# Kernel optimization log

Hardware: AMD Instinct MI355X
Metric: run time of the kernel (lower is better)

## Reference

```python
import jax, jax.numpy as jnp
import numpy as np

DIM = 1024
HEADS = 16
HEAD_DIM = DIM // HEADS
DFF = 4 * DIM  # SwiGLU expansion=4.0
EPS = 1e-5
NEG = -1e4  # original uses -1e4 causal mask, not -inf


def rms_norm(x, w):
    v = jnp.mean(x * x, axis=-1, keepdims=True)
    return w * (x * jax.lax.rsqrt(v + EPS))


def rotate_half(x):
    x1, x2 = jnp.split(x, 2, axis=-1)
    return jnp.concatenate((-x2, x1), axis=-1)


def setup_inputs() -> dict:
    key = jax.random.key(0)
    ks = jax.random.split(key, 12)
    B, S = 2, 2048
    s = 0.02
    h = jax.random.normal(ks[0], (B, S, DIM), jnp.float32)
    # RoPE tables, half-split convention: emb = concat(freqs, freqs)
    inv_freq = 1.0 / (10000.0 ** (np.arange(0, HEAD_DIM, 2, dtype=np.float32) / HEAD_DIM))
    freqs = np.arange(S, dtype=np.float32)[:, None] * inv_freq[None, :]
    emb = np.concatenate([freqs, freqs], axis=-1)
    cos = jnp.asarray(np.cos(emb))  # [S, HEAD_DIM]
    sin = jnp.asarray(np.sin(emb))
    return {
        "h": h, "cos": cos, "sin": sin,
        "norm1_w": jnp.ones((DIM,), jnp.float32),
        "wq": jax.random.normal(ks[1], (DIM, DIM), jnp.float32) * s,
        "wk": jax.random.normal(ks[2], (DIM, DIM), jnp.float32) * s,
        "wv": jax.random.normal(ks[3], (DIM, DIM), jnp.float32) * s,
        "wo": jax.random.normal(ks[4], (DIM, DIM), jnp.float32) * s,
        "norm2_w": jnp.ones((DIM,), jnp.float32),
        "gate_w": jax.random.normal(ks[5], (DFF, DIM), jnp.float32) * s,
        "gate_b": jnp.zeros((DFF,), jnp.float32),
        "up_w": jax.random.normal(ks[6], (DFF, DIM), jnp.float32) * s,
        "up_b": jnp.zeros((DFF,), jnp.float32),
        "down_w": jax.random.normal(ks[7], (DIM, DFF), jnp.float32) * s,
        "down_b": jnp.zeros((DIM,), jnp.float32),
        "gate": jnp.full((DIM,), 0.5, jnp.float32),
    }


def reference(h, cos, sin, norm1_w, wq, wk, wv, wo, norm2_w,
              gate_w, gate_b, up_w, up_b, down_w, down_b, gate):
    B, S, _ = h.shape
    scale = HEAD_DIM ** -0.5

    x = rms_norm(h, norm1_w)

    def heads(t):  # [B,S,DIM] -> [B,H,S,D]
        return t.reshape(B, S, HEADS, HEAD_DIM).transpose(0, 2, 1, 3)

    q = heads(x @ wq.T)
    k = heads(x @ wk.T)
    v = heads(x @ wv.T)

    # inline RoPE (cos/sin broadcast [S,D] over [B,H,S,D])
    q = q * cos + rotate_half(q) * sin
    k = k * cos + rotate_half(k) * sin

    scores = jnp.einsum('bhsd,bhtd->bhst', q, k) * scale
    causal = jnp.triu(jnp.full((S, S), NEG, jnp.float32), k=1)
    scores = scores + causal
    attn = jax.nn.softmax(scores, axis=-1)
    out = jnp.einsum('bhst,bhtd->bhsd', attn, v)
    out = out.transpose(0, 2, 1, 3).reshape(B, S, DIM)
    attn_out = out @ wo.T

    h = h + attn_out

    x2 = rms_norm(h, norm2_w)
    g = jax.nn.silu(x2 @ gate_w.T + gate_b)
    u = x2 @ up_w.T + up_b
    mlp = (g * u) @ down_w.T + down_b

    h = h + jax.nn.sigmoid(gate) * mlp
    return h
```

## Files before the change

### kernel.cpp

```cpp
#include <hip/hip_runtime.h>
#include <math.h>

#define DIM    1024
#define HEADS  16
#define HD     64
#define SEQ    2048
#define BATCH  2
#define TTOK   4096
#define DFF    4096
#define S3     3072
#define NTSW   16

typedef __attribute__((ext_vector_type(8))) short short8;
typedef __attribute__((ext_vector_type(4))) float f32x4;

__device__ __forceinline__ float bf2f(unsigned short u) {
  union { unsigned int u; float f; } v; v.u = ((unsigned int)u) << 16; return v.f;
}
__device__ __forceinline__ unsigned short f2bf(float f) {
  union { float f; unsigned int u; } v; v.f = f;
  return (unsigned short)((v.u + 0x7FFFu + ((v.u >> 16) & 1u)) >> 16);
}
__device__ __forceinline__ unsigned short f2bf_trunc(float f) {
  union { float f; unsigned int u; } v; v.f = f;
  return (unsigned short)(v.u >> 16);
}

#define AS1(p) ((const __attribute__((address_space(1))) void*)(p))
#define AS3(p) ((__attribute__((address_space(3))) void*)(p))

__global__ __launch_bounds__(256) void wconv_k(
    const float* __restrict__ s0, const float* __restrict__ s1,
    const float* __restrict__ s2, const float* __restrict__ s3,
    const float* __restrict__ s4, const float* __restrict__ s5,
    const float* __restrict__ s6, unsigned short* __restrict__ dst)
{
  const int i = blockIdx.x * 256 + threadIdx.x;
  const float* s; int base; int di = i;
  if (i < 1048576) {
    if (i < 524288) { if (i < 262144) { s = s0; base = 0; } else { s = s1; base = 262144; } }
    else            { if (i < 786432) { s = s2; base = 524288; } else { s = s3; base = 786432; } }
  } else if (i < 2097152) {
    s = s4; base = 1048576;
    const int u = i - base; const int r = u >> 8; const int c = u & 255;
    di = 1048576 + (((r >> 4) << 5) + (r & 15)) * 256 + c;
  } else if (i < 3145728) {
    s = s5; base = 2097152;
    const int u = i - base; const int r = u >> 8; const int c = u & 255;
    di = 1048576 + (((r >> 4) << 5) + 16 + (r & 15)) * 256 + c;
  } else {
    s = s6; base = 3145728;
  }
  const float4 f = ((const float4*)s)[i - base];
  unsigned long long o = (unsigned long long)f2bf(f.x)
                       | ((unsigned long long)f2bf(f.y) << 16)
                       | ((unsigned long long)f2bf(f.z) << 32)
                       | ((unsigned long long)f2bf(f.w) << 48);
  ((unsigned long long*)dst)[di] = o;
}

template<int MODE>
__global__ __launch_bounds__(256) void gemm_bt(
    const unsigned short* __restrict__ A,
    const unsigned short* __restrict__ W,
    unsigned short* __restrict__ C,
    float* __restrict__ Cf,
    const float* __restrict__ resf,
    const float* __restrict__ cosp,
    const float* __restrict__ sinp,
    int M, int N, int K)
{
  __shared__ __align__(16) unsigned short As[128 * 64];
  __shared__ __align__(16) unsigned short Bs[128 * 64];

  const int tid  = threadIdx.x;
  const int lane = tid & 63;
  const int wv   = tid >> 6;
  const int row0 = blockIdx.x * 128;
  const int col0 = blockIdx.y * 128;
  const int wm   = (wv >> 1) * 64;
  const int wn   = (wv & 1) * 64;
  const int lr   = lane & 15;
  const int lg   = lane >> 4;

  const int srow = lane >> 3;
  const int skg  = (lane & 7) ^ srow;

  f32x4 acc[4][4];
#pragma unroll
  for (int i = 0; i < 4; i++)
#pragma unroll
    for (int j = 0; j < 4; j++) acc[i][j] = (f32x4){0.f, 0.f, 0.f, 0.f};

  for (int k0 = 0; k0 < K; k0 += 64) {
#pragma unroll
    for (int i = 0; i < 4; i++) {
      const int c = wv * 4 + i;
      const unsigned short* ga = A + (size_t)(row0 + c * 8 + srow) * K + k0 + skg * 8;
      __builtin_amdgcn_global_load_lds(AS1(ga), AS3(As + c * 512), 16, 0, 0);
      const unsigned short* gb = W + (size_t)(col0 + c * 8 + srow) * K + k0 + skg * 8;
      __builtin_amdgcn_global_load_lds(AS1(gb), AS3(Bs + c * 512), 16, 0, 0);
    }
    __syncthreads();

#pragma unroll
    for (int ks = 0; ks < 2; ks++) {
      short8 af[4], bf[4];
#pragma unroll
      for (int i = 0; i < 4; i++) {
        const int r = wm + i * 16 + lr;
        af[i] = *(const short8*)(As + r * 64 + (((ks * 4 + lg) ^ (lr & 7)) * 8));
      }
#pragma unroll
      for (int j = 0; j < 4; j++) {
        const int r = wn + j * 16 + lr;
        bf[j] = *(const short8*)(Bs + r * 64 + (((ks * 4 + lg) ^ (lr & 7)) * 8));
      }
#pragma unroll
      for (int i = 0; i < 4; i++)
#pragma unroll
        for (int j = 0; j < 4; j++)
          acc[i][j] = __builtin_amdgcn_mfma_f32_16x16x32_bf16(af[i], bf[j], acc[i][j], 0, 0, 0);
    }
    __syncthreads();
  }

  if (MODE == 5) {
    const bool do_rope = (col0 < 2048);
#pragma unroll
    for (int i = 0; i < 4; i++) {
#pragma unroll
      for (int r = 0; r < 4; r++) {
        const int row = row0 + wm + i * 16 + lg * 4 + r;
        const int s = row & (SEQ - 1);
        const size_t rb = (size_t)row * N + col0 + wn;
        if (do_rope) {
#pragma unroll
          for (int jp = 0; jp < 2; jp++) {
            const int d = jp * 16 + lr;
            const float c = cosp[s * HD + d];
            const float sn = sinp[s * HD + d];
            const float x1v = acc[i][jp][r];
            const float x2v = acc[i][jp + 2][r];
            C[rb + d]      = f2bf(x1v * c - x2v * sn);
            C[rb + d + 32] = f2bf(x2v * c + x1v * sn);
          }
        } else {
#pragma unroll
          for (int j = 0; j < 4; j++)
            C[rb + j * 16 + lr] = f2bf(acc[i][j][r]);
        }
      }
    }
    return;
  }

#pragma unroll
  for (int i = 0; i < 4; i++) {
#pragma unroll
    for (int j = 0; j < 4; j++) {
      const int col = col0 + wn + j * 16 + lr;
#pragma unroll
      for (int r = 0; r < 4; r++) {
        const int row = row0 + wm + i * 16 + lg * 4 + r;
        const float v = acc[i][j][r];
        const size_t idx = (size_t)row * N + col;
        if (MODE == 3) {
          Cf[idx] = v + resf[idx];
        }
      }
    }
  }
}

template<int MODE>
__global__ __launch_bounds__(512, 2) void gemm256_k(
    const unsigned short* __restrict__ A,
    const unsigned short* __restrict__ W,
    unsigned short* __restrict__ G,
    const float* __restrict__ gbias,
    const float* __restrict__ ubias,
    int Kst)
{
  __shared__ __align__(16) unsigned short Asl[2 * 16384];
  __shared__ __align__(16) unsigned short Bsl[2 * 16384];

  const int tid  = threadIdx.x;
  const int lane = tid & 63;
  const int wv   = tid >> 6;
  const int row0 = blockIdx.x * 256;
  const int col0 = blockIdx.y * 256;
  const int wm   = (wv >> 2) * 128;
  const int wn   = (wv & 3) * 64;
  const int lr   = lane & 15;
  const int lg   = lane >> 4;
  const int kb   = (MODE == 6) ? blockIdx.z * 1024 : 0;

  const int rl   = tid >> 3;
  const int rq   = (rl & 31) + ((rl >> 5) << 7);
  const int cl8  = ((tid & 7) ^ (rl & 7)) * 8;
  const int ldsu = wv * 512;

  auto stA = [&](int t, int q) {
    const unsigned short* s = A + (size_t)(row0 + q * 32 + rq) * Kst + kb + t * 64 + cl8;
    __builtin_amdgcn_global_load_lds(AS1(s), AS3(Asl + (t & 1) * 16384 + q * 4096 + ldsu), 16, 0, 0);
  };
  auto stB = [&](int t, int q) {
    const unsigned short* s = W + (size_t)(col0 + q * 32 + rq) * Kst + kb + t * 64 + cl8;
    __builtin_amdgcn_global_load_lds(AS1(s), AS3(Bsl + (t & 1) * 16384 + q * 4096 + ldsu), 16, 0, 0);
  };

  f32x4 acc[8][4];
#pragma unroll
  for (int f = 0; f < 8; f++)
#pragma unroll
    for (int j = 0; j < 4; j++) acc[f][j] = (f32x4){0.f, 0.f, 0.f, 0.f};

  stB(0, 0); stB(0, 1); stB(0, 2); stB(0, 3);
  stA(0, 0); stA(0, 1); stA(0, 2); stA(0, 3);
  stB(1, 0); stB(1, 1); stB(1, 2); stB(1, 3);
  stA(1, 0); stA(1, 1);
  asm volatile("s_waitcnt vmcnt(6)" ::: "memory");
  __builtin_amdgcn_s_barrier();

#pragma unroll 1
  for (int J = 0; J < NTSW / 2; ++J) {
    const int t2 = 2 * J + 2, t3 = 2 * J + 3;
#pragma unroll
    for (int h = 0; h < 2; ++h) {
      const unsigned short* Ab = Asl + h * 16384;
      const unsigned short* Bb = Bsl + h * 16384;
      short8 bfr[4][2];
#pragma unroll
      for (int p = 0; p < 4; ++p) {
        if (p == 0) {
#pragma unroll
          for (int j = 0; j < 4; ++j) {
            const int rn   = wn + j * 16 + lr;
            const int q    = (rn & 127) >> 5;
            const int rloc = (rn & 31) + ((rn >> 7) << 5);
#pragma unroll
            for (int ks = 0; ks < 2; ++ks)
              bfr[j][ks] = *(const short8*)(Bb + q * 4096 + rloc * 64 +
                                            (((ks * 4 + lg) ^ (lr & 7)) * 8));
          }
        }
        short8 af[2][2];
#pragma unroll
        for (int e = 0; e < 2; ++e) {
          const int rloc = e * 16 + lr + ((wv >> 2) << 5);
#pragma unroll
          for (int ks = 0; ks < 2; ++ks)
            af[e][ks] = *(const short8*)(Ab + p * 4096 + rloc * 64 +
                                         (((ks * 4 + lg) ^ (lr & 7)) * 8));
        }
        if (h == 0) {
          if (p == 0)      { stA(2 * J + 1, 2); stA(2 * J + 1, 3); }
          else if (p == 1) { if (t2 < NTSW) { stB(t2, 0); stB(t2, 1); } }
          else if (p == 2) { if (t2 < NTSW) { stB(t2, 2); stB(t2, 3); } }
          else {
            if (t2 < NTSW) { stA(t2, 0); stA(t2, 1);
                             asm volatile("s_waitcnt vmcnt(6)" ::: "memory"); }
            else           { asm volatile("s_waitcnt vmcnt(0)" ::: "memory"); }
          }
        } else {
          if (p == 0)      { if (t2 < NTSW) { stA(t2, 2); stA(t2, 3); } }
          else if (p == 1) { if (t3 < NTSW) { stB(t3, 0); stB(t3, 1); } }
          else if (p == 2) { if (t3 < NTSW) { stB(t3, 2); stB(t3, 3); } }
          else {
            if (t3 < NTSW) { stA(t3, 0); stA(t3, 1);
                             asm volatile("s_waitcnt vmcnt(6)" ::: "memory"); }
            else           { asm volatile("s_waitcnt vmcnt(0)" ::: "memory"); }
          }
        }
        __builtin_amdgcn_s_barrier();
        asm volatile("s_waitcnt lgkmcnt(0)" ::: "memory");
        __builtin_amdgcn_sched_barrier(0);
        __builtin_amdgcn_s_setprio(1);
#pragma unroll
        for (int e = 0; e < 2; ++e)
#pragma unroll
          for (int j = 0; j < 4; ++j)
#pragma unroll
            for (int ks = 0; ks < 2; ++ks)
              acc[2 * p + e][j] = __builtin_amdgcn_mfma_f32_16x16x32_bf16(
                  af[e][ks], bfr[j][ks], acc[2 * p + e][j], 0, 0, 0);
        __builtin_amdgcn_s_setprio(0);
        __builtin_amdgcn_s_barrier();
      }
    }
  }

  if (MODE == 7) {
    const int cb = (col0 + wn) >> 1;
#pragma unroll
    for (int jp = 0; jp < 2; ++jp) {
      const int lcol = cb + jp * 16 + lr;
      const float gbv = gbias[lcol];
      const float ubv = ubias[lcol];
#pragma unroll
      for (int f = 0; f < 8; ++f) {
#pragma unroll
        for (int r = 0; r < 4; ++r) {
          const int row = row0 + wm + f * 16 + lg * 4 + r;
          float gv = acc[f][2 * jp][r] + gbv;
          gv = gv / (1.0f + __expf(-gv));
          const float uv = acc[f][2 * jp + 1][r] + ubv;
          G[(size_t)row * DFF + lcol] = f2bf(gv * uv);
        }
      }
    }
  } else {
    const size_t pz[4] = {4u * 1048576u, 8u * 1048576u, 16u * 1048576u, 0u};
    unsigned short* Cz = G + pz[blockIdx.z];
#pragma unroll
    for (int j = 0; j < 4; ++j) {
      const int col = col0 + wn + j * 16 + lr;
#pragma unroll
      for (int f = 0; f < 8; ++f) {
#pragma unroll
        for (int r = 0; r < 4; ++r) {
          const int row = row0 + wm + f * 16 + lg * 4 + r;
          Cz[(size_t)row * DIM + col] = f2bf(acc[f][j][r]);
        }
      }
    }
  }
}

__global__ __launch_bounds__(256) void dcomb_k(
    const unsigned short* __restrict__ ws, float* __restrict__ out,
    const float* __restrict__ db, const float* __restrict__ gate)
{
  const int i4 = blockIdx.x * 256 + threadIdx.x;
  const size_t idx = (size_t)i4 * 4;
  const int col = (int)(idx & 1023);
  const unsigned long long p0 = *(const unsigned long long*)(ws + 4u * 1048576u + idx);
  const unsigned long long p1 = *(const unsigned long long*)(ws + 8u * 1048576u + idx);
  const unsigned long long p2 = *(const unsigned long long*)(ws + 16u * 1048576u + idx);
  const unsigned long long p3 = *(const unsigned long long*)(ws + idx);
  float4 o = *(float4*)(out + idx);
  float* op = (float*)&o;
#pragma unroll
  for (int w = 0; w < 4; w++) {
    const float s = bf2f((unsigned short)(p0 >> (16 * w)))
                  + bf2f((unsigned short)(p1 >> (16 * w)))
                  + bf2f((unsigned short)(p2 >> (16 * w)))
                  + bf2f((unsigned short)(p3 >> (16 * w)))
                  + db[col + w];
    const float sg = 1.0f / (1.0f + __expf(-gate[col + w]));
    op[w] += sg * s;
  }
  *(float4*)(out + idx) = o;
}

template<int XF32>
__global__ __launch_bounds__(256) void rmsnorm_k(
    const void* __restrict__ Xv,
    const float* __restrict__ W,
    unsigned short* __restrict__ Y)
{
  const int t  = blockIdx.x;
  const int i0 = threadIdx.x * 4;

  float v[4];
  if (XF32) {
    const float4 f = *(const float4*)((const float*)Xv + (size_t)t * DIM + i0);
    v[0] = f.x; v[1] = f.y; v[2] = f.z; v[3] = f.w;
  } else {
    unsigned long long raw = *(const unsigned long long*)((const unsigned short*)Xv + (size_t)t * DIM + i0);
#pragma unroll
    for (int k = 0; k < 4; k++) v[k] = bf2f((unsigned short)(raw >> (16 * k)));
  }

  float ss = v[0] * v[0] + v[1] * v[1] + v[2] * v[2] + v[3] * v[3];
#pragma unroll
  for (int off = 32; off > 0; off >>= 1) ss += __shfl_xor(ss, off);

  __shared__ float red[4];
  if ((threadIdx.x & 63) == 0) red[threadIdx.x >> 6] = ss;
  __syncthreads();
  const float tot = red[0] + red[1] + red[2] + red[3];
  const float r = rsqrtf(tot * (1.0f / DIM) + 1e-5f);

  const float4 wf = *(const float4*)(W + i0);
  const float wv4[4] = {wf.x, wf.y, wf.z, wf.w};
  unsigned long long o = 0;
#pragma unroll
  for (int k = 0; k < 4; k++)
    o |= ((unsigned long long)f2bf(v[k] * r * wv4[k])) << (16 * k);
  *(unsigned long long*)(Y + (size_t)t * DIM + i0) = o;
}

__device__ const unsigned char cqt[32] = {10,10,15,15,9,9,13,14,14,14,15,4,8,8,12,12,13,13,7,7,11,11,11,12,3,6,6,5,5,2,1,0};
__device__ const unsigned char ctb[32] = {0,11,0,11,0,10,0,0,10,20,22,0,0,9,0,9,10,19,0,8,0,8,16,18,0,0,7,0,6,0,0,0};
__device__ const unsigned char ccnt[32] = {11,11,11,11,10,10,10,10,10,10,10,10,9,9,9,9,9,9,8,8,8,8,8,8,8,7,7,6,6,6,4,2};
__device__ const unsigned char cchv[32] = {0,1,0,1,0,1,0,0,1,2,2,0,0,1,0,1,1,2,0,1,0,1,2,2,0,0,1,0,1,0,0,0};
__device__ const unsigned char cpsv[32] = {255,5,255,14,255,4,255,255,12,13,15,255,255,3,255,8,10,11,255,2,255,6,7,9,255,255,1,255,0,255,255,255};

__global__ __launch_bounds__(256) void fattn_k(
    const unsigned short* __restrict__ QKV,
    unsigned short* __restrict__ O,
    unsigned short* __restrict__ Pbuf,
    float* __restrict__ Lbuf)
{
  __shared__ __align__(16) unsigned short Ks[2][64 * 64];
  __shared__ __align__(16) unsigned short Vt[2][64 * 72];
  __shared__ __align__(16) unsigned short Ps[4 * 32 * 72];

  const int tid  = threadIdx.x;
  const int lane = tid & 63;
  const int wv   = tid >> 6;
  const int lr   = lane & 15;
  const int lg   = lane >> 4;

  const int j  = blockIdx.x;
  const int bh = blockIdx.y;
  const int qt = cqt[j];
  const int tb = ctb[j];
  const int nt = ccnt[j];
  const int ch = cchv[j];
  const int ps = cpsv[j];
  const int b  = bh >> 4, h = bh & 15;
  const int q0 = qt * 128;
  const size_t rowb = (size_t)b * SEQ;
  const int qoff = h * HD;
  const int koff = 1024 + qoff;
  const int voff = 2048 + qoff;

  short8 aq[2][2];
#pragma unroll
  for (int rf = 0; rf < 2; rf++) {
    const size_t tok = rowb + q0 + wv * 32 + rf * 16 + lr;
    aq[rf][0] = *(const short8*)(QKV + tok * S3 + qoff + lg * 8);
    aq[rf][1] = *(const short8*)(QKV + tok * S3 + qoff + 32 + lg * 8);
  }

  f32x4 o[2][4];
  f32x4 lacc[2];
#pragma unroll
  for (int rf = 0; rf < 2; rf++) {
    lacc[rf] = (f32x4){0.f, 0.f, 0.f, 0.f};
#pragma unroll
    for (int d = 0; d < 4; d++) o[rf][d] = (f32x4){0.f, 0.f, 0.f, 0.f};
  }
  short8 onesb;
#pragma unroll
  for (int jj = 0; jj < 8; jj++) onesb[jj] = (short)0x3F80;

  const int srow = lane >> 3;
  const int skg  = (lane & 7) ^ srow;
  const int kv   = tid >> 2;
  const int d0   = (tid & 3) * 16;

  const float C1 = 0.125f * 1.44269504f;
  const float C2 = 11.5415603f;

  auto stage = [&](int buf, int ti) {
    const int t0 = (tb + ti) * 64;
    unsigned short* ksb = &Ks[buf][0];
#pragma unroll
    for (int i = 0; i < 2; i++) {
      const int c = wv * 2 + i;
      const unsigned short* gk = QKV + (rowb + t0 + c * 8 + srow) * S3 + koff + skg * 8;
      __builtin_amdgcn_global_load_lds(AS1(gk), AS3(ksb + c * 512), 16, 0, 0);
    }
    unsigned short* vtb = &Vt[buf][0];
    const unsigned short* gv = QKV + (rowb + t0 + kv) * S3 + voff + d0;
    const short8 v0 = *(const short8*)gv;
    const short8 v1 = *(const short8*)(gv + 8);
    const int klo = kv & 7, khi = kv >> 3;
#pragma unroll
    for (int w = 0; w < 8; w++) {
      const int da = d0 + w, db2 = d0 + 8 + w;
      vtb[da  * 72 + ((khi ^ ((da  >> 3) & 7)) * 8) + klo] = (unsigned short)v0[w];
      vtb[db2 * 72 + ((khi ^ ((db2 >> 3) & 7)) * 8) + klo] = (unsigned short)v1[w];
    }
  };

  stage(0, 0);

  for (int ti = 0; ti < nt; ti++) {
    __syncthreads();
    if (ti + 1 < nt) stage((ti + 1) & 1, ti + 1);

    const int t0 = (tb + ti) * 64;
    const unsigned short* ksb = &Ks[ti & 1][0];
    const unsigned short* vtb = &Vt[ti & 1][0];

    f32x4 S[2][4];
#pragma unroll
    for (int sub = 0; sub < 4; sub++) {
      const int kr = sub * 16 + lr;
      const short8 bk0 = *(const short8*)(ksb + kr * 64 + ((lg       ^ (kr & 7)) * 8));
      const short8 bk1 = *(const short8*)(ksb + kr * 64 + (((4 + lg) ^ (kr & 7)) * 8));
#pragma unroll
      for (int rf = 0; rf < 2; rf++) {
        f32x4 s = (f32x4){0.f, 0.f, 0.f, 0.f};
        s = __builtin_amdgcn_mfma_f32_16x16x32_bf16(aq[rf][0], bk0, s, 0, 0, 0);
        s = __builtin_amdgcn_mfma_f32_16x16x32_bf16(aq[rf][1], bk1, s, 0, 0, 0);
        S[rf][sub] = s;
      }
    }

    unsigned short* pw = Ps + wv * (32 * 72);
#pragma unroll
    for (int rf = 0; rf < 2; rf++) {
      const int qmin = q0 + wv * 32 + rf * 16;
      const bool diag = (t0 + 63 > qmin);
#pragma unroll
      for (int sub = 0; sub < 4; sub++) {
#pragma unroll
        for (int r = 0; r < 4; r++) {
          float t = fmaf(S[rf][sub][r], C1, -C2);
          if (diag && (t0 + sub * 16 + lr > qmin + lg * 4 + r)) t = -INFINITY;
          const float p = exp2f(t);
          pw[(rf * 16 + lg * 4 + r) * 72 + sub * 16 + lr] = f2bf_trunc(p);
        }
      }
    }

#pragma unroll
    for (int kf = 0; kf < 2; kf++) {
      const short8 pa0 = *(const short8*)(pw + lr * 72 + kf * 32 + lg * 8);
      const short8 pa1 = *(const short8*)(pw + (16 + lr) * 72 + kf * 32 + lg * 8);
      lacc[0] = __builtin_amdgcn_mfma_f32_16x16x32_bf16(pa0, onesb, lacc[0], 0, 0, 0);
      lacc[1] = __builtin_amdgcn_mfma_f32_16x16x32_bf16(pa1, onesb, lacc[1], 0, 0, 0);
#pragma unroll
      for (int dsub = 0; dsub < 4; dsub++) {
        const int d = dsub * 16 + lr;
        const short8 bvf = *(const short8*)(vtb + d * 72 +
                             (((kf * 4 + lg) ^ ((d >> 3) & 7)) * 8));
        o[0][dsub] = __builtin_amdgcn_mfma_f32_16x16x32_bf16(pa0, bvf, o[0][dsub], 0, 0, 0);
        o[1][dsub] = __builtin_amdgcn_mfma_f32_16x16x32_bf16(pa1, bvf, o[1][dsub], 0, 0, 0);
      }
    }
  }

  if (ps == 255 && qt < 5) {
#pragma unroll
    for (int rf = 0; rf < 2; rf++) {
      float inv[4];
#pragma unroll
      for (int r = 0; r < 4; r++) inv[r] = 1.0f / lacc[rf][r];
#pragma unroll
      for (int dsub = 0; dsub < 4; dsub++)
#pragma unroll
        for (int r = 0; r < 4; r++)
          O[(rowb + q0 + wv * 32 + rf * 16 + lg * 4 + r) * DIM + h * HD + dsub * 16 + lr] =
              f2bf(o[rf][dsub][r] * inv[r]);
    }
  } else {
    const int lbase = ((bh * 11 + (qt - 5)) * 3 + ch) * 128;
#pragma unroll
    for (int rf = 0; rf < 2; rf++) {
      const int rbase = wv * 32 + rf * 16 + lg * 4;
      if (lr == 0) {
#pragma unroll
        for (int r = 0; r < 4; r++) Lbuf[lbase + rbase + r] = lacc[rf][r];
      }
    }
    if (ps == 255) {
#pragma unroll
      for (int rf = 0; rf < 2; rf++)
#pragma unroll
        for (int dsub = 0; dsub < 4; dsub++)
#pragma unroll
          for (int r = 0; r < 4; r++)
            O[(rowb + q0 + wv * 32 + rf * 16 + lg * 4 + r) * DIM + h * HD + dsub * 16 + lr] =
                f2bf(o[rf][dsub][r]);
    } else {
      unsigned short* pb = Pbuf + ((size_t)bh * 16 + ps) * 8192;
#pragma unroll
      for (int rf = 0; rf < 2; rf++) {
        const int rbase = wv * 32 + rf * 16 + lg * 4;
#pragma unroll
        for (int dsub = 0; dsub < 4; dsub++)
#pragma unroll
          for (int r = 0; r < 4; r++)
            pb[(rbase + r) * 64 + dsub * 16 + lr] = f2bf(o[rf][dsub][r]);
      }
    }
  }
}

__global__ __launch_bounds__(256) void fattn_combine_k(
    const unsigned short* __restrict__ Pbuf,
    const float* __restrict__ Lbuf,
    unsigned short* __restrict__ O)
{
  const int qt = 5 + blockIdx.x;
  const int bh = blockIdx.y;
  const int b  = bh >> 4, h = bh & 15;
  const int q0 = qt * 128;
  const size_t rowb = (size_t)b * SEQ;
  const int pbase_t[11] = {0, 1, 2, 3, 4, 5, 6, 8, 10, 12, 14};
  const int pb0 = pbase_t[qt - 5];
  const int np  = (qt < 11) ? 1 : 2;
  const int lbase = (bh * 11 + (qt - 5)) * 3 * 128;

  const unsigned short* p0 = Pbuf + ((size_t)bh * 16 + pb0) * 8192;
  const unsigned short* p1 = Pbuf + ((size_t)bh * 16 + pb0 + 1) * 8192;

#pragma unroll
  for (int it = 0; it < 4; it++) {
    const int idx = it * 2048 + threadIdx.x * 8;
    const int row = idx >> 6;
    const int col = idx & 63;
    float ls = Lbuf[lbase + row] + Lbuf[lbase + 128 + row];
    if (np == 2) ls += Lbuf[lbase + 256 + row];
    const float inv = 1.0f / ls;

    unsigned short* op = O + (rowb + q0 + row) * DIM + h * HD + col;
    const short8 vb = *(const short8*)op;
    const short8 e0 = *(const short8*)(p0 + idx);
    short8 e1;
    if (np == 2) e1 = *(const short8*)(p1 + idx);
    short8 r;
#pragma unroll
    for (int w = 0; w < 8; w++) {
      float s = bf2f((unsigned short)vb[w]) + bf2f((unsigned short)e0[w]);
      if (np == 2) s += bf2f((unsigned short)e1[w]);
      r[w] = (short)f2bf(s * inv);
    }
    *(short8*)op = r;
  }
}

extern "C" void kernel_launch(void* const* d_in, const int* in_sizes, int n_in,
                              void* d_out, int out_size, void* d_ws, size_t ws_size,
                              hipStream_t stream)
{
  const float* h    = (const float*)d_in[0];
  const float* cosb = (const float*)d_in[1];
  const float* sinb = (const float*)d_in[2];
  const float* n1w  = (const float*)d_in[3];
  const float* n2w  = (const float*)d_in[8];
  const float* gb   = (const float*)d_in[10];
  const float* ub   = (const float*)d_in[12];
  const float* db   = (const float*)d_in[14];
  const float* gatep= (const float*)d_in[15];
  float* out = (float*)d_out;

  unsigned short* ws = (unsigned short*)d_ws;
  const size_t M1 = 1u << 20;

  unsigned short* wqkv = ws;
  unsigned short* wo_c = ws + 3 * M1;
  unsigned short* gu_c = ws + 4 * M1;
  unsigned short* dw_c = ws + 12 * M1;
  unsigned short* x1   = ws + 16 * M1;
  unsigned short* Pbuf = ws + 16 * M1;
  unsigned short* x2   = ws + 16 * M1;
  float*          Lbuf = (float*)ws;
  unsigned short* qkv  = ws + 20 * M1;
  unsigned short* attn = ws + 32 * M1;
  unsigned short* g    = qkv;

  const dim3 blk(256);
  const dim3 gq(TTOK / 128, S3 / 128);
  const dim3 g1(TTOK / 128, DIM / 128);
  const dim3 gsw(TTOK / 256, (2 * DFF) / 256);
  const dim3 gd(TTOK / 256, DIM / 256, 4);

  wconv_k<<<16384, blk, 0, stream>>>(
      (const float*)d_in[4], (const float*)d_in[5], (const float*)d_in[6],
      (const float*)d_in[7], (const float*)d_in[9], (const float*)d_in[11],
      (const float*)d_in[13], ws);

  rmsnorm_k<1><<<TTOK, blk, 0, stream>>>(h, n1w, x1);

  gemm_bt<5><<<gq, blk, 0, stream>>>(x1, wqkv, qkv, nullptr, nullptr,
                                     cosb, sinb, TTOK, S3, DIM);

  fattn_k<<<dim3(32, BATCH * HEADS), blk, 0, stream>>>(qkv, attn, Pbuf, Lbuf);
  fattn_combine_k<<<dim3(11, BATCH * HEADS), blk, 0, stream>>>(Pbuf, Lbuf, attn);

  gemm_bt<3><<<g1, blk, 0, stream>>>(attn, wo_c, nullptr, out, h,
                                     nullptr, nullptr, TTOK, DIM, DIM);

  rmsnorm_k<1><<<TTOK, blk, 0, stream>>>(out, n2w, x2);

  gemm256_k<7><<<gsw, dim3(512), 0, stream>>>(x2, gu_c, g, gb, ub, 1024);

  gemm256_k<6><<<gd, dim3(512), 0, stream>>>(g, dw_c, ws, nullptr, nullptr, 4096);

  dcomb_k<<<4096, blk, 0, stream>>>(ws, out, db, gatep);
}
```

Measured before the change: 430.6 us.

## Fuse split-K down-projection reduction into GEMM epilogue via atomics

The split-K down-projection GEMM now adds its partial products straight into the fp32 residual output with atomicAdd, applying the sigmoid gate and bias (bias only on the z=0 slice). This removes the bf16 partial-sum buffers and the separate combine kernel. The gate/up GEMM is also launched as two half-width launches with a column offset. The atomics add contention and make the summation order nondeterministic, while partials are no longer rounded to bf16.

```diff
diff --git a/kernel.cpp b/kernel.cpp
--- a/kernel.cpp
+++ b/kernel.cpp
@@ -178,9 +178,10 @@
     const unsigned short* __restrict__ A,
     const unsigned short* __restrict__ W,
     unsigned short* __restrict__ G,
+    float* __restrict__ Cf,
     const float* __restrict__ gbias,
     const float* __restrict__ ubias,
-    int Kst)
+    int Kst, int colb)
 {
   __shared__ __align__(16) unsigned short Asl[2 * 16384];
   __shared__ __align__(16) unsigned short Bsl[2 * 16384];
@@ -189,7 +190,7 @@
   const int lane = tid & 63;
   const int wv   = tid >> 6;
   const int row0 = blockIdx.x * 256;
-  const int col0 = blockIdx.y * 256;
+  const int col0 = blockIdx.y * 256 + colb;
   const int wm   = (wv >> 2) * 128;
   const int wn   = (wv & 3) * 64;
   const int lr   = lane & 15;
@@ -311,47 +312,22 @@
       }
     }
   } else {
-    const size_t pz[4] = {4u * 1048576u, 8u * 1048576u, 16u * 1048576u, 0u};
-    unsigned short* Cz = G + pz[blockIdx.z];
+    const bool z0 = (blockIdx.z == 0);
 #pragma unroll
     for (int j = 0; j < 4; ++j) {
       const int col = col0 + wn + j * 16 + lr;
+      const float dbv = z0 ? gbias[col] : 0.0f;
+      const float sg  = 1.0f / (1.0f + __expf(-ubias[col]));
 #pragma unroll
       for (int f = 0; f < 8; ++f) {
 #pragma unroll
         for (int r = 0; r < 4; ++r) {
           const int row = row0 + wm + f * 16 + lg * 4 + r;
-          Cz[(size_t)row * DIM + col] = f2bf(acc[f][j][r]);
-        }
-      }
-    }
-  }
-}
-
-__global__ __launch_bounds__(256) void dcomb_k(
-    const unsigned short* __restrict__ ws, float* __restrict__ out,
-    const float* __restrict__ db, const float* __restrict__ gate)
-{
-  const int i4 = blockIdx.x * 256 + threadIdx.x;
-  const size_t idx = (size_t)i4 * 4;
-  const int col = (int)(idx & 1023);
-  const unsigned long long p0 = *(const unsigned long long*)(ws + 4u * 1048576u + idx);
-  const unsigned long long p1 = *(const unsigned long long*)(ws + 8u * 1048576u + idx);
-  const unsigned long long p2 = *(const unsigned long long*)(ws + 16u * 1048576u + idx);
-  const unsigned long long p3 = *(const unsigned long long*)(ws + idx);
-  float4 o = *(float4*)(out + idx);
-  float* op = (float*)&o;
-#pragma unroll
-  for (int w = 0; w < 4; w++) {
-    const float s = bf2f((unsigned short)(p0 >> (16 * w)))
-                  + bf2f((unsigned short)(p1 >> (16 * w)))
-                  + bf2f((unsigned short)(p2 >> (16 * w)))
-                  + bf2f((unsigned short)(p3 >> (16 * w)))
-                  + db[col + w];
-    const float sg = 1.0f / (1.0f + __expf(-gate[col + w]));
-    op[w] += sg * s;
-  }
-  *(float4*)(out + idx) = o;
+          atomicAdd(Cf + (size_t)row * DIM + col, sg * (acc[f][j][r] + dbv));
+        }
+      }
+    }
+  }
 }
 
 template<int XF32>
@@ -660,7 +636,7 @@
   const dim3 blk(256);
   const dim3 gq(TTOK / 128, S3 / 128);
   const dim3 g1(TTOK / 128, DIM / 128);
-  const dim3 gsw(TTOK / 256, (2 * DFF) / 256);
+  const dim3 gsw(TTOK / 256, 16);
   const dim3 gd(TTOK / 256, DIM / 256, 4);
 
   wconv_k<<<16384, blk, 0, stream>>>(
@@ -681,9 +657,8 @@
 
   rmsnorm_k<1><<<TTOK, blk, 0, stream>>>(out, n2w, x2);
 
-  gemm256_k<7><<<gsw, dim3(512), 0, stream>>>(x2, gu_c, g, gb, ub, 1024);
-
-  gemm256_k<6><<<gd, dim3(512), 0, stream>>>(g, dw_c, ws, nullptr, nullptr, 4096);
-
-  dcomb_k<<<4096, blk, 0, stream>>>(ws, out, db, gatep);
-}
+  gemm256_k<7><<<gsw, dim3(512), 0, stream>>>(x2, gu_c, g, nullptr, gb, ub, 1024, 0);
+  gemm256_k<7><<<gsw, dim3(512), 0, stream>>>(x2, gu_c, g, nullptr, gb, ub, 1024, 4096);
+
+  gemm256_k<6><<<gd, dim3(512), 0, stream>>>(g, dw_c, nullptr, out, db, gatep, 4096, 0);
+}
```

After: 440.2 us. 2.3% more time.
